# Kernel tuning notes

Measured on AMD Instinct MI355X. Metric: run time of the kernel, lower is better.

## Reference

```python
import jax, jax.numpy as jnp
import numpy as np

B, N, K, H, D = 2, 8192, 16, 4, 32
C_IN, C_OUT = 64, 128
HD = H * D


def setup_inputs() -> dict:
    key = jax.random.key(0)
    ks = jax.random.split(key, 16)
    s = 0.02
    return {
        "xyzs": jax.random.normal(ks[0], (B, N, 3), jnp.float32),
        "features": jax.random.normal(ks[1], (B, N, C_IN), jnp.float32),
        "k_graph": jax.random.randint(ks[2], (B, N, K), 0, N),
        # projections (stored as [in, out]; torch Linear applies x @ W.T)
        "Wk": jax.random.normal(ks[3], (C_IN, HD), jnp.float32) * s,
        "Wv": jax.random.normal(ks[4], (C_IN, HD), jnp.float32) * s,
        "Wq": jax.random.normal(ks[5], (C_IN, HD), jnp.float32) * s,
        # aggregate MLP: Linear(HD,HD) -> ReLU -> Linear(HD,H)
        "A1": jax.random.normal(ks[6], (HD, HD), jnp.float32) * s,
        "b1": jnp.zeros((HD,), jnp.float32),
        "A2": jax.random.normal(ks[7], (HD, H), jnp.float32) * s,
        "b2": jnp.zeros((H,), jnp.float32),
        # position MLP: Linear(3,3) -> ReLU -> Linear(3,HD)
        "P1": jax.random.normal(ks[8], (3, 3), jnp.float32) * s,
        "bp1": jnp.zeros((3,), jnp.float32),
        "P2": jax.random.normal(ks[9], (3, HD), jnp.float32) * s,
        "bp2": jnp.zeros((HD,), jnp.float32),
        # output projection Linear(HD, C_OUT)
        "Wout": jax.random.normal(ks[10], (HD, C_OUT), jnp.float32) * s,
        "bout": jnp.zeros((C_OUT,), jnp.float32),
    }


def reference(xyzs, features, k_graph, Wk, Wv, Wq, A1, b1, A2, b2,
              P1, bp1, P2, bp2, Wout, bout):
    # KNN gather (irregular access): [B,N,K,*]
    nbr_feat = jax.vmap(lambda f, g: f[g])(features, k_graph)   # [B,N,K,C_IN]
    nbr_xyz = jax.vmap(lambda x, g: x[g])(xyzs, k_graph)        # [B,N,K,3]

    rel_pos = xyzs[:, :, None, :] - nbr_xyz                      # [B,N,K,3]
    pe = jax.nn.relu(rel_pos @ P1 + bp1) @ P2 + bp2              # [B,N,K,HD]

    keys = nbr_feat @ Wk                                         # [B,N,K,HD]
    values = nbr_feat @ Wv                                       # [B,N,K,HD]
    queries = features @ Wq                                      # [B,N,HD]

    # subtraction attention + aggregate MLP -> per-head logits
    attn = queries[:, :, None, :] - keys + pe                    # [B,N,K,HD]
    attn = jax.nn.relu(attn @ A1 + b1) @ A2 + b2                 # [B,N,K,H]
    attn = jax.nn.softmax(attn, axis=-2)                         # softmax over K

    # weighted reduce over neighbors
    fv = (values + pe).reshape(B, N, K, H, D)
    fused = jnp.sum(attn[..., None] * fv, axis=2)                # [B,N,H,D]
    fused = fused.reshape(B, N, HD)
    return fused @ Wout + bout                                   # [B,N,C_OUT]
```

## Files before the change

### kernel.cpp

```cpp
#include <hip/hip_runtime.h>
#include <hip/hip_bf16.h>

#define BATCH 2
#define NPTS  8192
#define BN    (BATCH * NPTS)
#define KNN   16
#define HEADS 4
#define HD    128
#define CIN   64
#define COUT  128
#define WCOLS 384

using short8  = __attribute__((ext_vector_type(8))) short;
using float4v = __attribute__((ext_vector_type(4))) float;

static __device__ __forceinline__ unsigned short f2bf(float x) {
    unsigned u = __float_as_uint(x);
    u += 0x7fffu + ((u >> 16) & 1u);
    return (unsigned short)(u >> 16);
}
static __device__ __forceinline__ float bf_lo(unsigned u) { return __uint_as_float(u << 16); }
static __device__ __forceinline__ float bf_hi(unsigned u) { return __uint_as_float(u & 0xffff0000u); }
static __device__ __forceinline__ unsigned pack2(float a, float b) {
    return (unsigned)f2bf(a) | ((unsigned)f2bf(b) << 16);
}

template <int CTRL>
static __device__ __forceinline__ float dpp_mov(float x) {
    return __int_as_float(
        __builtin_amdgcn_update_dpp(0, __float_as_int(x), CTRL, 0xf, 0xf, false));
}
static __device__ __forceinline__ float ror_sum16(float x) {
    x += dpp_mov<0x128>(x);
    x += dpp_mov<0x124>(x);
    x += dpp_mov<0x122>(x);
    x += dpp_mov<0x121>(x);
    return x;
}
static __device__ __forceinline__ float ror_max16(float x) {
    x = fmaxf(x, dpp_mov<0x128>(x));
    x = fmaxf(x, dpp_mov<0x124>(x));
    x = fmaxf(x, dpp_mov<0x122>(x));
    x = fmaxf(x, dpp_mov<0x121>(x));
    return x;
}

__global__ void prep_kernel(const float* __restrict__ Wk,
                            const float* __restrict__ Wv,
                            const float* __restrict__ Wq,
                            const float* __restrict__ A1,
                            const float* __restrict__ b1,
                            const float* __restrict__ P2,
                            const float* __restrict__ bp2,
                            const float* __restrict__ Wout,
                            unsigned short* __restrict__ WcatT,
                            unsigned short* __restrict__ WoutT,
                            float* __restrict__ P2A1,
                            float* __restrict__ cvec) {
    int t = blockIdx.x * blockDim.x + threadIdx.x;
    if (t < WCOLS * CIN) {
        int n = t >> 6, kk = t & 63;
        float val;
        if (n < 2 * HD) {
            const float* w = (n < HD ? Wq : Wk) + kk * HD;
            int jj = n & (HD - 1);
            float acc = 0.f;
            #pragma unroll 4
            for (int m = 0; m < HD; m += 4) {
                float4 wr = *(const float4*)(w + m);
                acc += wr.x * A1[(m+0)*HD + jj] + wr.y * A1[(m+1)*HD + jj]
                     + wr.z * A1[(m+2)*HD + jj] + wr.w * A1[(m+3)*HD + jj];
            }
            val = acc;
        } else {
            val = Wv[kk * HD + (n - 2 * HD)];
        }
        WcatT[t] = f2bf(val);
    } else if (t < WCOLS * CIN + COUT * HD) {
        int u = t - WCOLS * CIN;
        int n = u >> 7, kk = u & 127;
        WoutT[u] = f2bf(Wout[kk * COUT + n]);
    } else if (t < WCOLS * CIN + COUT * HD + 3 * HD) {
        int u = t - (WCOLS * CIN + COUT * HD);
        int r = u / HD, j = u % HD;
        const float* w = P2 + r * HD;
        float acc = 0.f;
        #pragma unroll 4
        for (int m = 0; m < HD; m += 4) {
            float4 wr = *(const float4*)(w + m);
            acc += wr.x * A1[(m+0)*HD + j] + wr.y * A1[(m+1)*HD + j]
                 + wr.z * A1[(m+2)*HD + j] + wr.w * A1[(m+3)*HD + j];
        }
        P2A1[u] = acc;
    } else if (t < WCOLS * CIN + COUT * HD + 3 * HD + HD) {
        int j = t - (WCOLS * CIN + COUT * HD + 3 * HD);
        float acc = b1[j];
        #pragma unroll 4
        for (int m = 0; m < HD; m += 4) {
            float4 wr = *(const float4*)(bp2 + m);
            acc += wr.x * A1[(m+0)*HD + j] + wr.y * A1[(m+1)*HD + j]
                 + wr.z * A1[(m+2)*HD + j] + wr.w * A1[(m+3)*HD + j];
        }
        cvec[j] = acc;
    }
}

#define AK 88
__global__ __launch_bounds__(256) void qkv_kernel(const float* __restrict__ F,
                                                  const unsigned short* __restrict__ WcatT,
                                                  const float* __restrict__ cvec,
                                                  unsigned short* __restrict__ QKVb) {
    __shared__ unsigned short Af[64 * AK];
    __shared__ unsigned short Bf[WCOLS * AK];
    int p0 = blockIdx.x * 64;
    int t = threadIdx.x;

    #pragma unroll
    for (int i = 0; i < 4; ++i) {
        int v = t + i * 256;
        int row = v >> 4, c4 = (v & 15) * 4;
        float4 fa = *(const float4*)(F + (p0 + row) * CIN + c4);
        uint2 u = make_uint2(pack2(fa.x, fa.y), pack2(fa.z, fa.w));
        *(uint2*)(&Af[row * AK + c4]) = u;
    }
    #pragma unroll
    for (int i = 0; i < 12; ++i) {
        int v = t + i * 256;
        int n = v >> 3, j16 = v & 7;
        *(uint4*)(&Bf[n * AK + j16 * 8]) = ((const uint4*)WcatT)[v];
    }
    __syncthreads();

    int w = t >> 6, l = t & 63;
    int ml = l & 15, quad = l >> 4;
    int m0 = w * 16;

    short8 a0 = *(const short8*)(&Af[(m0 + ml) * AK + quad * 8]);
    short8 a1 = *(const short8*)(&Af[(m0 + ml) * AK + 32 + quad * 8]);

    #pragma unroll
    for (int nt = 0; nt < 24; ++nt) {
        short8 b0 = *(const short8*)(&Bf[(nt * 16 + ml) * AK + quad * 8]);
        short8 b1 = *(const short8*)(&Bf[(nt * 16 + ml) * AK + 32 + quad * 8]);
        float4v acc = {0.f, 0.f, 0.f, 0.f};
        acc = __builtin_amdgcn_mfma_f32_16x16x32_bf16(a0, b0, acc, 0, 0, 0);
        acc = __builtin_amdgcn_mfma_f32_16x16x32_bf16(a1, b1, acc, 0, 0, 0);
        int n = nt * 16 + ml;
        float cadd = (n < HD) ? cvec[n] : 0.f;
        #pragma unroll
        for (int r = 0; r < 4; ++r) {
            int row = p0 + m0 + quad * 4 + r;
            QKVb[row * WCOLS + n] = f2bf(acc[r] + cadd);
        }
    }
}

__global__ __launch_bounds__(256) void attn_kernel(
        const float* __restrict__ xyzs, const int* __restrict__ kg,
        const unsigned short* __restrict__ QKVb,
        const float* __restrict__ P1, const float* __restrict__ bp1,
        const float* __restrict__ P2, const float* __restrict__ bp2,
        const float* __restrict__ P2A1,
        const float* __restrict__ A2, const float* __restrict__ b2,
        unsigned short* __restrict__ FUSEDb) {
    int p = blockIdx.x;
    int b = p >> 13;
    int t = threadIdx.x;
    int g = t >> 4, k = t & 15, c0 = g * 8;
    int w = t >> 6;
    int lane = t & 63;

    __shared__ float4 A2s[HD];
    __shared__ float4 lgp[4][16];
    __shared__ float4 hs16[16];
    __shared__ float  ats[64];
    __shared__ float4 hbf[4];

    if (t < HD) A2s[t] = *(const float4*)(A2 + t * 4);

    int idx = kg[p * KNN + k];
    int q = b * NPTS + idx;

    float r0 = xyzs[p*3+0] - xyzs[q*3+0];
    float r1 = xyzs[p*3+1] - xyzs[q*3+1];
    float r2 = xyzs[p*3+2] - xyzs[q*3+2];
    float h0 = fmaxf(r0*P1[0] + r1*P1[3] + r2*P1[6] + bp1[0], 0.f);
    float h1 = fmaxf(r0*P1[1] + r1*P1[4] + r2*P1[7] + bp1[1], 0.f);
    float h2 = fmaxf(r0*P1[2] + r1*P1[5] + r2*P1[8] + bp1[2], 0.f);
    if (g == 0) hs16[k] = make_float4(h0, h1, h2, 0.f);

    uint4 qu = *(const uint4*)(QKVb + p * WCOLS + c0);
    uint4 ku = *(const uint4*)(QKVb + q * WCOLS + HD + c0);
    uint4 vu = *(const uint4*)(QKVb + q * WCOLS + 2 * HD + c0);

    float qz[8] = { bf_lo(qu.x), bf_hi(qu.x), bf_lo(qu.y), bf_hi(qu.y),
                    bf_lo(qu.z), bf_hi(qu.z), bf_lo(qu.w), bf_hi(qu.w) };
    float kr[8] = { bf_lo(ku.x), bf_hi(ku.x), bf_lo(ku.y), bf_hi(ku.y),
                    bf_lo(ku.z), bf_hi(ku.z), bf_lo(ku.w), bf_hi(ku.w) };

    float wa0[8], wa1[8], wa2[8];
    *(float4*)(wa0)     = *(const float4*)(P2A1 + 0*HD + c0);
    *(float4*)(wa0 + 4) = *(const float4*)(P2A1 + 0*HD + c0 + 4);
    *(float4*)(wa1)     = *(const float4*)(P2A1 + 1*HD + c0);
    *(float4*)(wa1 + 4) = *(const float4*)(P2A1 + 1*HD + c0 + 4);
    *(float4*)(wa2)     = *(const float4*)(P2A1 + 2*HD + c0);
    *(float4*)(wa2 + 4) = *(const float4*)(P2A1 + 2*HD + c0 + 4);

    __syncthreads();

    float pl0 = 0.f, pl1 = 0.f, pl2 = 0.f, pl3 = 0.f;
    #pragma unroll
    for (int j = 0; j < 8; ++j) {
        float z = fmaxf(qz[j] - kr[j] + h0*wa0[j] + h1*wa1[j] + h2*wa2[j], 0.f);
        float4 ar = A2s[c0 + j];
        pl0 += z * ar.x; pl1 += z * ar.y; pl2 += z * ar.z; pl3 += z * ar.w;
    }
    pl0 += __shfl_xor(pl0, 16, 64); pl0 += __shfl_xor(pl0, 32, 64);
    pl1 += __shfl_xor(pl1, 16, 64); pl1 += __shfl_xor(pl1, 32, 64);
    pl2 += __shfl_xor(pl2, 16, 64); pl2 += __shfl_xor(pl2, 32, 64);
    pl3 += __shfl_xor(pl3, 16, 64); pl3 += __shfl_xor(pl3, 32, 64);
    if (lane < 16) lgp[w][lane] = make_float4(pl0, pl1, pl2, pl3);
    __syncthreads();

    if (t < 64) {
        int hh = t >> 4, kk = t & 15;
        const float* lp = (const float*)lgp;
        float lgt = b2[hh] + lp[0*64 + kk*4 + hh] + lp[1*64 + kk*4 + hh]
                           + lp[2*64 + kk*4 + hh] + lp[3*64 + kk*4 + hh];
        float m = ror_max16(lgt);
        float e = __expf(lgt - m);
        float s = ror_sum16(e);
        float a = e / s;
        ats[t] = a;
        float4 hv = hs16[kk];
        float hb0 = ror_sum16(a * hv.x);
        float hb1 = ror_sum16(a * hv.y);
        float hb2 = ror_sum16(a * hv.z);
        if (kk == 0) hbf[hh] = make_float4(hb0, hb1, hb2, 0.f);
    }
    __syncthreads();

    float a = ats[w * 16 + k];
    float vr[8] = { bf_lo(vu.x), bf_hi(vu.x), bf_lo(vu.y), bf_hi(vu.y),
                    bf_lo(vu.z), bf_hi(vu.z), bf_lo(vu.w), bf_hi(vu.w) };
    float wv[8];
    #pragma unroll
    for (int j = 0; j < 8; ++j) wv[j] = ror_sum16(a * vr[j]);

    if (k == 0) {
        float4 hb = hbf[w];
        float q0[8], q1[8], q2[8], bpv[8];
        *(float4*)(q0)     = *(const float4*)(P2 + 0*HD + c0);
        *(float4*)(q0 + 4) = *(const float4*)(P2 + 0*HD + c0 + 4);
        *(float4*)(q1)     = *(const float4*)(P2 + 1*HD + c0);
        *(float4*)(q1 + 4) = *(const float4*)(P2 + 1*HD + c0 + 4);
        *(float4*)(q2)     = *(const float4*)(P2 + 2*HD + c0);
        *(float4*)(q2 + 4) = *(const float4*)(P2 + 2*HD + c0 + 4);
        *(float4*)(bpv)     = *(const float4*)(bp2 + c0);
        *(float4*)(bpv + 4) = *(const float4*)(bp2 + c0 + 4);
        float f[8];
        #pragma unroll
        for (int j = 0; j < 8; ++j)
            f[j] = wv[j] + hb.x*q0[j] + hb.y*q1[j] + hb.z*q2[j] + bpv[j];
        uint4 fu;
        fu.x = pack2(f[0], f[1]); fu.y = pack2(f[2], f[3]);
        fu.z = pack2(f[4], f[5]); fu.w = pack2(f[6], f[7]);
        *(uint4*)(FUSEDb + p * HD + c0) = fu;
    }
}

#define OK2 144
__global__ __launch_bounds__(256) void out_kernel(const unsigned short* __restrict__ FUSEDb,
                                                  const unsigned short* __restrict__ WoutT,
                                                  const float* __restrict__ bout,
                                                  float* __restrict__ out) {
    __shared__ unsigned short Af[64 * OK2];
    __shared__ unsigned short Bf[HD * OK2];
    int p0 = blockIdx.x * 64;
    int t = threadIdx.x;

    #pragma unroll
    for (int i = 0; i < 4; ++i) {
        int v = t + i * 256;
        int row = v >> 4, j16 = v & 15;
        *(uint4*)(&Af[row * OK2 + j16 * 8]) = ((const uint4*)FUSEDb)[(p0 + row) * 16 + j16];
    }
    #pragma unroll
    for (int i = 0; i < 8; ++i) {
        int v = t + i * 256;
        int n = v >> 4, j16 = v & 15;
        *(uint4*)(&Bf[n * OK2 + j16 * 8]) = ((const uint4*)WoutT)[v];
    }
    __syncthreads();

    int w = t >> 6, l = t & 63;
    int ml = l & 15, quad = l >> 4;
    int m0 = w * 16;

    short8 af[4];
    #pragma unroll
    for (int ks = 0; ks < 4; ++ks)
        af[ks] = *(const short8*)(&Af[(m0 + ml) * OK2 + ks * 32 + quad * 8]);

    #pragma unroll
    for (int nt = 0; nt < 8; ++nt) {
        float4v acc = {0.f, 0.f, 0.f, 0.f};
        #pragma unroll
        for (int ks = 0; ks < 4; ++ks) {
            short8 bf = *(const short8*)(&Bf[(nt * 16 + ml) * OK2 + ks * 32 + quad * 8]);
            acc = __builtin_amdgcn_mfma_f32_16x16x32_bf16(af[ks], bf, acc, 0, 0, 0);
        }
        int n = nt * 16 + ml;
        float bo = bout[n];
        #pragma unroll
        for (int r = 0; r < 4; ++r) {
            int row = p0 + m0 + quad * 4 + r;
            out[row * COUT + n] = acc[r] + bo;
        }
    }
}

extern "C" void kernel_launch(void* const* d_in, const int* in_sizes, int n_in,
                              void* d_out, int out_size, void* d_ws, size_t ws_size,
                              hipStream_t stream) {
    const float* xyzs = (const float*)d_in[0];
    const float* feat = (const float*)d_in[1];
    const int*   kg   = (const int*)  d_in[2];
    const float* Wk   = (const float*)d_in[3];
    const float* Wv   = (const float*)d_in[4];
    const float* Wq   = (const float*)d_in[5];
    const float* A1   = (const float*)d_in[6];
    const float* b1   = (const float*)d_in[7];
    const float* A2   = (const float*)d_in[8];
    const float* b2   = (const float*)d_in[9];
    const float* P1   = (const float*)d_in[10];
    const float* bp1  = (const float*)d_in[11];
    const float* P2   = (const float*)d_in[12];
    const float* bp2  = (const float*)d_in[13];
    const float* Wout = (const float*)d_in[14];
    const float* bout = (const float*)d_in[15];
    float* out = (float*)d_out;

    float* ws = (float*)d_ws;
    float* cvec = ws;
    float* P2A1 = ws + 128;
    unsigned short* QKVb  = (unsigned short*)(ws + 512);
    unsigned short* FUSEDb = QKVb + (size_t)BN * WCOLS;
    unsigned short* WcatT = FUSEDb + (size_t)BN * HD;
    unsigned short* WoutT = WcatT + WCOLS * CIN;

    int prep_elems = WCOLS*CIN + COUT*HD + 3*HD + HD;
    prep_kernel<<<(prep_elems + 255) / 256, 256, 0, stream>>>(
        Wk, Wv, Wq, A1, b1, P2, bp2, Wout, WcatT, WoutT, P2A1, cvec);

    qkv_kernel<<<BN / 64, 256, 0, stream>>>(feat, WcatT, cvec, QKVb);

    attn_kernel<<<BN, 256, 0, stream>>>(
        xyzs, kg, QKVb, P1, bp1, P2, bp2, P2A1, A2, b2, FUSEDb);

    out_kernel<<<BN / 64, 256, 0, stream>>>(FUSEDb, WoutT, bout, out);
}
```

Measured before the change: 158.4 us.

## Load weights directly into registers and swap MFMA operands for vectorized stores

The qkv and output GEMM kernels no longer stage the full weight matrix in shared memory. Each wave now loads its own column slice of weights straight from global into registers and loops over all four 16-row tiles. MFMA operands are swapped so each lane holds four consecutive output columns, which allows packed uint2 and float4 stores instead of scattered scalar stores. The prep kernel is reorganised so each wave handles one weight row with coalesced lane access. This cuts LDS footprint and traffic and improves occupancy and store coalescing, at the cost of higher register pressure and repeated global weight loads that rely on the cache.

```diff
diff --git a/kernel.cpp b/kernel.cpp
--- a/kernel.cpp
+++ b/kernel.cpp
@@ -45,62 +45,48 @@
     return x;
 }
 
-__global__ void prep_kernel(const float* __restrict__ Wk,
-                            const float* __restrict__ Wv,
-                            const float* __restrict__ Wq,
-                            const float* __restrict__ A1,
-                            const float* __restrict__ b1,
-                            const float* __restrict__ P2,
-                            const float* __restrict__ bp2,
-                            const float* __restrict__ Wout,
-                            unsigned short* __restrict__ WcatT,
-                            unsigned short* __restrict__ WoutT,
-                            float* __restrict__ P2A1,
-                            float* __restrict__ cvec) {
-    int t = blockIdx.x * blockDim.x + threadIdx.x;
-    if (t < WCOLS * CIN) {
-        int n = t >> 6, kk = t & 63;
-        float val;
-        if (n < 2 * HD) {
-            const float* w = (n < HD ? Wq : Wk) + kk * HD;
+__global__ __launch_bounds__(256) void prep_kernel(
+        const float* __restrict__ Wk, const float* __restrict__ Wv,
+        const float* __restrict__ Wq, const float* __restrict__ A1,
+        const float* __restrict__ b1, const float* __restrict__ P2,
+        const float* __restrict__ bp2, const float* __restrict__ Wout,
+        unsigned short* __restrict__ WcatT, unsigned short* __restrict__ WoutT,
+        float* __restrict__ P2A1, float* __restrict__ cvec) {
+    int W = blockIdx.x * 4 + (threadIdx.x >> 6);
+    int lane = threadIdx.x & 63;
+    if (W < 384) {
+        int kk = W / 6, nb = W % 6;
+        int n = nb * 64 + lane;
+        if (nb < 4) {
+            const float* src = (nb < 2 ? Wq : Wk) + kk * HD;
             int jj = n & (HD - 1);
             float acc = 0.f;
-            #pragma unroll 4
-            for (int m = 0; m < HD; m += 4) {
-                float4 wr = *(const float4*)(w + m);
-                acc += wr.x * A1[(m+0)*HD + jj] + wr.y * A1[(m+1)*HD + jj]
-                     + wr.z * A1[(m+2)*HD + jj] + wr.w * A1[(m+3)*HD + jj];
-            }
-            val = acc;
+            #pragma unroll 8
+            for (int m = 0; m < HD; ++m)
+                acc += src[m] * A1[m * HD + jj];
+            WcatT[n * CIN + kk] = f2bf(acc);
         } else {
-            val = Wv[kk * HD + (n - 2 * HD)];
+            WcatT[n * CIN + kk] = f2bf(Wv[kk * HD + (n - 2 * HD)]);
         }
-        WcatT[t] = f2bf(val);
-    } else if (t < WCOLS * CIN + COUT * HD) {
-        int u = t - WCOLS * CIN;
+    } else if (W < 384 + 256) {
+        int u = (W - 384) * 64 + lane;
         int n = u >> 7, kk = u & 127;
         WoutT[u] = f2bf(Wout[kk * COUT + n]);
-    } else if (t < WCOLS * CIN + COUT * HD + 3 * HD) {
-        int u = t - (WCOLS * CIN + COUT * HD);
-        int r = u / HD, j = u % HD;
-        const float* w = P2 + r * HD;
+    } else if (W < 646) {
+        int u = (W - 640) * 64 + lane;
+        int r = u >> 7, j = u & 127;
+        const float* src = P2 + r * HD;
         float acc = 0.f;
-        #pragma unroll 4
-        for (int m = 0; m < HD; m += 4) {
-            float4 wr = *(const float4*)(w + m);
-            acc += wr.x * A1[(m+0)*HD + j] + wr.y * A1[(m+1)*HD + j]
-                 + wr.z * A1[(m+2)*HD + j] + wr.w * A1[(m+3)*HD + j];
-        }
+        #pragma unroll 8
+        for (int m = 0; m < HD; ++m)
+            acc += src[m] * A1[m * HD + j];
         P2A1[u] = acc;
-    } else if (t < WCOLS * CIN + COUT * HD + 3 * HD + HD) {
-        int j = t - (WCOLS * CIN + COUT * HD + 3 * HD);
+    } else {
+        int j = (W - 646) * 64 + lane;
         float acc = b1[j];
-        #pragma unroll 4
-        for (int m = 0; m < HD; m += 4) {
-            float4 wr = *(const float4*)(bp2 + m);
-            acc += wr.x * A1[(m+0)*HD + j] + wr.y * A1[(m+1)*HD + j]
-                 + wr.z * A1[(m+2)*HD + j] + wr.w * A1[(m+3)*HD + j];
-        }
+        #pragma unroll 8
+        for (int m = 0; m < HD; ++m)
+            acc += bp2[m] * A1[m * HD + j];
         cvec[j] = acc;
     }
 }
@@ -111,7 +97,6 @@
                                                   const float* __restrict__ cvec,
                                                   unsigned short* __restrict__ QKVb) {
     __shared__ unsigned short Af[64 * AK];
-    __shared__ unsigned short Bf[WCOLS * AK];
     int p0 = blockIdx.x * 64;
     int t = threadIdx.x;
 
@@ -120,37 +105,45 @@
         int v = t + i * 256;
         int row = v >> 4, c4 = (v & 15) * 4;
         float4 fa = *(const float4*)(F + (p0 + row) * CIN + c4);
-        uint2 u = make_uint2(pack2(fa.x, fa.y), pack2(fa.z, fa.w));
-        *(uint2*)(&Af[row * AK + c4]) = u;
-    }
-    #pragma unroll
-    for (int i = 0; i < 12; ++i) {
-        int v = t + i * 256;
-        int n = v >> 3, j16 = v & 7;
-        *(uint4*)(&Bf[n * AK + j16 * 8]) = ((const uint4*)WcatT)[v];
+        *(uint2*)(&Af[row * AK + c4]) = make_uint2(pack2(fa.x, fa.y), pack2(fa.z, fa.w));
     }
     __syncthreads();
 
     int w = t >> 6, l = t & 63;
     int ml = l & 15, quad = l >> 4;
-    int m0 = w * 16;
-
-    short8 a0 = *(const short8*)(&Af[(m0 + ml) * AK + quad * 8]);
-    short8 a1 = *(const short8*)(&Af[(m0 + ml) * AK + 32 + quad * 8]);
-
-    #pragma unroll
-    for (int nt = 0; nt < 24; ++nt) {
-        short8 b0 = *(const short8*)(&Bf[(nt * 16 + ml) * AK + quad * 8]);
-        short8 b1 = *(const short8*)(&Bf[(nt * 16 + ml) * AK + 32 + quad * 8]);
-        float4v acc = {0.f, 0.f, 0.f, 0.f};
-        acc = __builtin_amdgcn_mfma_f32_16x16x32_bf16(a0, b0, acc, 0, 0, 0);
-        acc = __builtin_amdgcn_mfma_f32_16x16x32_bf16(a1, b1, acc, 0, 0, 0);
-        int n = nt * 16 + ml;
-        float cadd = (n < HD) ? cvec[n] : 0.f;
-        #pragma unroll
-        for (int r = 0; r < 4; ++r) {
-            int row = p0 + m0 + quad * 4 + r;
-            QKVb[row * WCOLS + n] = f2bf(acc[r] + cadd);
+    int n0 = w * 96;
+
+    short8 b[6][2];
+    #pragma unroll
+    for (int j = 0; j < 6; ++j) {
+        int n = n0 + j * 16 + ml;
+        b[j][0] = *(const short8*)(WcatT + n * CIN + quad * 8);
+        b[j][1] = *(const short8*)(WcatT + n * CIN + 32 + quad * 8);
+    }
+    short8 a[4][2];
+    #pragma unroll
+    for (int mt = 0; mt < 4; ++mt) {
+        a[mt][0] = *(const short8*)(&Af[(mt * 16 + ml) * AK + quad * 8]);
+        a[mt][1] = *(const short8*)(&Af[(mt * 16 + ml) * AK + 32 + quad * 8]);
+    }
+
+    #pragma unroll
+    for (int j = 0; j < 6; ++j) {
+        #pragma unroll
+        for (int mt = 0; mt < 4; ++mt) {
+            float4v acc = {0.f, 0.f, 0.f, 0.f};
+            acc = __builtin_amdgcn_mfma_f32_16x16x32_bf16(b[j][0], a[mt][0], acc, 0, 0, 0);
+            acc = __builtin_amdgcn_mfma_f32_16x16x32_bf16(b[j][1], a[mt][1], acc, 0, 0, 0);
+            int nc = n0 + j * 16 + quad * 4;
+            float c0 = 0.f, c1 = 0.f, c2 = 0.f, c3 = 0.f;
+            if (nc < HD) {
+                float4 cv = *(const float4*)(cvec + nc);
+                c0 = cv.x; c1 = cv.y; c2 = cv.z; c3 = cv.w;
+            }
+            int row = p0 + mt * 16 + ml;
+            *(uint2*)(QKVb + row * WCOLS + nc) =
+                make_uint2(pack2(acc[0] + c0, acc[1] + c1),
+                           pack2(acc[2] + c2, acc[3] + c3));
         }
     }
 }
@@ -275,47 +268,49 @@
                                                   const float* __restrict__ bout,
                                                   float* __restrict__ out) {
     __shared__ unsigned short Af[64 * OK2];
-    __shared__ unsigned short Bf[HD * OK2];
     int p0 = blockIdx.x * 64;
     int t = threadIdx.x;
 
     #pragma unroll
     for (int i = 0; i < 4; ++i) {
         int v = t + i * 256;
-        int row = v >> 4, j16 = v & 15;
-        *(uint4*)(&Af[row * OK2 + j16 * 8]) = ((const uint4*)FUSEDb)[(p0 + row) * 16 + j16];
-    }
-    #pragma unroll
-    for (int i = 0; i < 8; ++i) {
-        int v = t + i * 256;
-        int n = v >> 4, j16 = v & 15;
-        *(uint4*)(&Bf[n * OK2 + j16 * 8]) = ((const uint4*)WoutT)[v];
+        int row = v >> 4, c8 = (v & 15) * 8;
+        *(uint4*)(&Af[row * OK2 + c8]) = *(const uint4*)(FUSEDb + (p0 + row) * HD + c8);
     }
     __syncthreads();
 
     int w = t >> 6, l = t & 63;
     int ml = l & 15, quad = l >> 4;
-    int m0 = w * 16;
-
-    short8 af[4];
-    #pragma unroll
-    for (int ks = 0; ks < 4; ++ks)
-        af[ks] = *(const short8*)(&Af[(m0 + ml) * OK2 + ks * 32 + quad * 8]);
-
-    #pragma unroll
-    for (int nt = 0; nt < 8; ++nt) {
-        float4v acc = {0.f, 0.f, 0.f, 0.f};
-        #pragma unroll
-        for (int ks = 0; ks < 4; ++ks) {
-            short8 bf = *(const short8*)(&Bf[(nt * 16 + ml) * OK2 + ks * 32 + quad * 8]);
-            acc = __builtin_amdgcn_mfma_f32_16x16x32_bf16(af[ks], bf, acc, 0, 0, 0);
-        }
-        int n = nt * 16 + ml;
-        float bo = bout[n];
-        #pragma unroll
-        for (int r = 0; r < 4; ++r) {
-            int row = p0 + m0 + quad * 4 + r;
-            out[row * COUT + n] = acc[r] + bo;
+    int n0 = w * 32;
+
+    short8 b[2][4];
+    #pragma unroll
+    for (int j = 0; j < 2; ++j) {
+        int n = n0 + j * 16 + ml;
+        #pragma unroll
+        for (int ks = 0; ks < 4; ++ks)
+            b[j][ks] = *(const short8*)(WoutT + n * HD + ks * 32 + quad * 8);
+    }
+    short8 a[4][4];
+    #pragma unroll
+    for (int mt = 0; mt < 4; ++mt)
+        #pragma unroll
+        for (int ks = 0; ks < 4; ++ks)
+            a[mt][ks] = *(const short8*)(&Af[(mt * 16 + ml) * OK2 + ks * 32 + quad * 8]);
+
+    #pragma unroll
+    for (int j = 0; j < 2; ++j) {
+        int nc = n0 + j * 16 + quad * 4;
+        float4 bo = *(const float4*)(bout + nc);
+        #pragma unroll
+        for (int mt = 0; mt < 4; ++mt) {
+            float4v acc = {0.f, 0.f, 0.f, 0.f};
+            #pragma unroll
+            for (int ks = 0; ks < 4; ++ks)
+                acc = __builtin_amdgcn_mfma_f32_16x16x32_bf16(b[j][ks], a[mt][ks], acc, 0, 0, 0);
+            int row = p0 + mt * 16 + ml;
+            *(float4*)(out + row * COUT + nc) =
+                make_float4(acc[0] + bo.x, acc[1] + bo.y, acc[2] + bo.z, acc[3] + bo.w);
         }
     }
 }
@@ -349,8 +344,7 @@
     unsigned short* WcatT = FUSEDb + (size_t)BN * HD;
     unsigned short* WoutT = WcatT + WCOLS * CIN;
 
-    int prep_elems = WCOLS*CIN + COUT*HD + 3*HD + HD;
-    prep_kernel<<<(prep_elems + 255) / 256, 256, 0, stream>>>(
+    prep_kernel<<<162, 256, 0, stream>>>(
         Wk, Wv, Wq, A1, b1, P2, bp2, Wout, WcatT, WoutT, P2A1, cvec);
 
     qkv_kernel<<<BN / 64, 256, 0, stream>>>(feat, WcatT, cvec, QKVb);
```

After: 161.8 us. 2.2% more time.
